# Kernel tuning notes

Measured on AMD Instinct MI355X. Metric: run time of the kernel, lower is better.

## Reference

```python
import jax, jax.numpy as jnp
import numpy as np

ANG_Y, ANG_X = 3, 3
ST = ANG_Y * ANG_X
K = 9                      # square kernel
OH, OW = 128, 128          # output_size
IN_C, OUT_C = 3, 3
H, W = 384, 384
B = 4


def setup_inputs() -> dict:
    key = jax.random.key(0)
    k_lf, = jax.random.split(key, 1)
    lf = jax.random.uniform(k_lf, (B, ST, IN_C, H, W), dtype=jnp.float32)
    # Learned locally-connected weights: one (out_c, in_c, OH, OW, K*K) tensor
    # per angular position, initialized as the center-tap identity (as in __init__).
    weights = jnp.zeros((ST, OUT_C, IN_C, OH, OW, K * K), dtype=jnp.float32)
    center = (K * K) // 2
    ch = jnp.arange(IN_C)
    weights = weights.at[:, ch, ch, :, :, center].set(1.0)
    biases = jnp.zeros((ST, OUT_C, OH, OW), dtype=jnp.float32)
    return {"lf": lf, "weights": weights, "biases": biases}


def reference(lf, weights, biases):
    b, st, c, h, w = lf.shape
    dh, dw = ANG_Y, ANG_X  # unfold stride
    # Padding exactly as in linear_filter
    pad_x = (OW - 1) * ANG_X + (K - w)
    pad_right = pad_x // 2
    pad_left = pad_x - pad_right
    pad_y = (OH - 1) * ANG_Y + (K - h)
    pad_bottom = pad_y // 2
    pad_top = pad_y - pad_bottom
    padded = jnp.pad(
        lf, ((0, 0), (0, 0), (0, 0), (pad_top, pad_bottom), (pad_left, pad_right))
    )
    # Extract K x K windows with stride (dh, dw), vectorized over batch and
    # all angular positions at once (replaces the triple Python loop).
    rows = jnp.arange(OH) * dh          # (OH,)
    cols = jnp.arange(OW) * dw          # (OW,)
    koff = jnp.arange(K)                # (K,)
    p = padded[:, :, :, rows[:, None] + koff[None, :], :]          # (b,st,c,OH,K,Wp)
    p = p[:, :, :, :, :, cols[:, None] + koff[None, :]]            # (b,st,c,OH,K,OW,K)
    p = p.transpose(0, 1, 2, 3, 5, 4, 6).reshape(b, st, c, OH, OW, K * K)
    # Locally-connected (unshared-weight) conv: per-angular, per-pixel weights.
    out = jnp.einsum("bsihwk,soihwk->bsohw", p, weights) + biases[None]
    return jnp.clip(out, 0.0, 1.0)
```

## Files before the change

### kernel.cpp

```cpp
#include <hip/hip_runtime.h>


#define ST 9
#define INC 3
#define OUTC 3
#define OHH 128
#define OWW 128
#define KDIM 9
#define KK 81
#define HH 384
#define WW 384
#define HWSZ (HH*WW)
#define WQ 16
#define SLICE (WQ*KK)

typedef float f32x4 __attribute__((ext_vector_type(4)));
struct __attribute__((packed, aligned(4))) U4 { f32x4 v; };

__device__ __forceinline__ void gll16(const float* g, float* l) {
  __builtin_amdgcn_global_load_lds((const __attribute__((address_space(1))) void*)g,
                                   (__attribute__((address_space(3))) void*)l, 16, 0, 0);
}

__global__ __launch_bounds__(128) void lf_filter_kernel(
    const float* __restrict__ lf, const float* __restrict__ wts,
    const float* __restrict__ bias, float* __restrict__ out)
{
  __shared__ __align__(16) float ldsW[OUTC][SLICE];

  const int t   = threadIdx.x;
  const int wl  = t & 15;
  const int b   = (t >> 4) & 3;
  const int kh  = t >> 6;
  const int bid = blockIdx.x;
  const int wg  = bid & 7;
  const int h   = (bid >> 3) & 127;
  const int s   = bid >> 10;
  const int w   = wg*WQ + wl;
  const int xbase = 3*w - 3;
  const int ybase = 3*h - 3;

  const int  base  = xbase < 0 ? 0 : (xbase > WW-KDIM ? WW-KDIM : xbase);
  const bool s_neg = (xbase < base);
  const bool s_pos = (xbase > base);

  const float* lfb = lf + (size_t)(b*ST + s)*INC*HWSZ;
  const int wu = (t & ~63) * 4;

  const int ky0 = kh ? 5 : 0;
  const int ky1 = kh ? 9 : 5;

  float acc[OUTC] = {0.f, 0.f, 0.f};

  #pragma unroll 1
  for (int i = 0; i < INC; ++i) {
    __syncthreads();

    #pragma unroll
    for (int o = 0; o < OUTC; ++o) {
      const float* wsrc = wts + ((size_t)(((s*OUTC + o)*INC + i)*OHH + h)*OWW + wg*WQ)*KK;
      float* dst = ldsW[o];
      #pragma unroll
      for (int j = 0; j < 2; ++j)
        gll16(wsrc + (size_t)(j*128 + t)*4, dst + j*512 + wu);
      if (t < 68)
        gll16(wsrc + (size_t)(256 + t)*4, dst + 1024 + wu);
    }
    __syncthreads();

    const float* lfr = lfb + (size_t)i*HWSZ;
    const int wb = wl*KK;
    #pragma unroll 1
    for (int ky = ky0; ky < ky1; ++ky) {
      const int y = ybase + ky;
      if ((unsigned)y < (unsigned)HH) {
        const float* rp = lfr + (size_t)y*WW + base;
        const f32x4 va = reinterpret_cast<const U4*>(rp)->v;
        const f32x4 vb = reinterpret_cast<const U4*>(rp + 4)->v;
        const float rc = rp[8];
        const float raw[KDIM] = {va.x, va.y, va.z, va.w, vb.x, vb.y, vb.z, vb.w, rc};
        float lv[KDIM];
        #pragma unroll
        for (int kx = 0; kx < KDIM; ++kx) {
          const float nv = (kx >= 3) ? raw[kx-3] : 0.f;
          const float pv = (kx <= 5) ? raw[kx+3] : 0.f;
          lv[kx] = s_neg ? nv : (s_pos ? pv : raw[kx]);
        }
        #pragma unroll
        for (int o = 0; o < OUTC; ++o) {
          const float* wrow = &ldsW[o][wb + ky*KDIM];
          float a = acc[o];
          #pragma unroll
          for (int kx = 0; kx < KDIM; ++kx)
            a = fmaf(lv[kx], wrow[kx], a);
          acc[o] = a;
        }
      }
    }
  }

  float* part = (float*)ldsW;
  __syncthreads();
  if (kh == 1) {
    const int q = t & 63;
    #pragma unroll
    for (int o = 0; o < OUTC; ++o) part[q*3 + o] = acc[o];
  }
  __syncthreads();
  if (kh == 0) {
    #pragma unroll
    for (int o = 0; o < OUTC; ++o) {
      const float bv = bias[((s*OUTC + o)*OHH + h)*OWW + w];
      float r = acc[o] + part[t*3 + o] + bv;
      r = r < 0.f ? 0.f : (r > 1.f ? 1.f : r);
      out[(((size_t)(b*ST + s)*OUTC + o)*OHH + h)*OWW + w] = r;
    }
  }
}

extern "C" void kernel_launch(void* const* d_in, const int* in_sizes, int n_in,
                              void* d_out, int out_size, void* d_ws, size_t ws_size,
                              hipStream_t stream) {
  const float* lf   = (const float*)d_in[0];
  const float* wts  = (const float*)d_in[1];
  const float* bias = (const float*)d_in[2];
  float* out = (float*)d_out;
  dim3 grid(ST * OHH * 8);
  dim3 block(128);
  hipLaunchKernelGGL(lf_filter_kernel, grid, block, 0, stream, lf, wts, bias, out);
}
```

Before: 99.97 us.

## Halve per-block width tile, split kernel rows four ways, and swizzle block order

Each block now covers 8 output columns instead of 16 and splits the 9 kernel rows across four thread groups (2,2,2,3) rather than two, doubling the grid. The LDS weight slice is halved and the cross-group reduction now sums three partial buffers. Block indices are also remapped so consecutive launched blocks stride across the grid, which spreads work and memory traffic across XCDs. The goal is more parallelism and shorter per-thread serial loops, at the cost of more blocks, more reduction traffic and less reuse of weight loads.

```diff
diff --git a/kernel.cpp b/kernel.cpp
--- a/kernel.cpp
+++ b/kernel.cpp
@@ -11,8 +11,9 @@
 #define HH 384
 #define WW 384
 #define HWSZ (HH*WW)
-#define WQ 16
+#define WQ 8
 #define SLICE (WQ*KK)
+#define NWG (ST*OHH*16)
 
 typedef float f32x4 __attribute__((ext_vector_type(4)));
 struct __attribute__((packed, aligned(4))) U4 { f32x4 v; };
@@ -29,13 +30,14 @@
   __shared__ __align__(16) float ldsW[OUTC][SLICE];
 
   const int t   = threadIdx.x;
-  const int wl  = t & 15;
-  const int b   = (t >> 4) & 3;
-  const int kh  = t >> 6;
-  const int bid = blockIdx.x;
-  const int wg  = bid & 7;
-  const int h   = (bid >> 3) & 127;
-  const int s   = bid >> 10;
+  const int wl  = t & 7;
+  const int b   = (t >> 3) & 3;
+  const int kq  = t >> 5;
+  const int raw = blockIdx.x;
+  const int bid = (raw & 7) * (NWG/8) + (raw >> 3);
+  const int wg  = bid & 15;
+  const int h   = (bid >> 4) & 127;
+  const int s   = bid >> 11;
   const int w   = wg*WQ + wl;
   const int xbase = 3*w - 3;
   const int ybase = 3*h - 3;
@@ -47,8 +49,8 @@
   const float* lfb = lf + (size_t)(b*ST + s)*INC*HWSZ;
   const int wu = (t & ~63) * 4;
 
-  const int ky0 = kh ? 5 : 0;
-  const int ky1 = kh ? 9 : 5;
+  const int kyA = kq*2;
+  const int nky = (kq == 3) ? 3 : 2;
 
   float acc[OUTC] = {0.f, 0.f, 0.f};
 
@@ -60,35 +62,35 @@
     for (int o = 0; o < OUTC; ++o) {
       const float* wsrc = wts + ((size_t)(((s*OUTC + o)*INC + i)*OHH + h)*OWW + wg*WQ)*KK;
       float* dst = ldsW[o];
-      #pragma unroll
-      for (int j = 0; j < 2; ++j)
-        gll16(wsrc + (size_t)(j*128 + t)*4, dst + j*512 + wu);
-      if (t < 68)
-        gll16(wsrc + (size_t)(256 + t)*4, dst + 1024 + wu);
+      gll16(wsrc + (size_t)t*4, dst + wu);
+      if (t < 34)
+        gll16(wsrc + (size_t)(128 + t)*4, dst + 512 + wu);
     }
     __syncthreads();
 
     const float* lfr = lfb + (size_t)i*HWSZ;
     const int wb = wl*KK;
     #pragma unroll 1
-    for (int ky = ky0; ky < ky1; ++ky) {
-      const int y = ybase + ky;
+    for (int r = 0; r < nky; ++r) {
+      const int ky = kyA + r;
+      const int y  = ybase + ky;
       if ((unsigned)y < (unsigned)HH) {
         const float* rp = lfr + (size_t)y*WW + base;
         const f32x4 va = reinterpret_cast<const U4*>(rp)->v;
         const f32x4 vb = reinterpret_cast<const U4*>(rp + 4)->v;
         const float rc = rp[8];
-        const float raw[KDIM] = {va.x, va.y, va.z, va.w, vb.x, vb.y, vb.z, vb.w, rc};
+        const float raw9[KDIM] = {va.x, va.y, va.z, va.w, vb.x, vb.y, vb.z, vb.w, rc};
         float lv[KDIM];
         #pragma unroll
         for (int kx = 0; kx < KDIM; ++kx) {
-          const float nv = (kx >= 3) ? raw[kx-3] : 0.f;
-          const float pv = (kx <= 5) ? raw[kx+3] : 0.f;
-          lv[kx] = s_neg ? nv : (s_pos ? pv : raw[kx]);
+          const float nv = (kx >= 3) ? raw9[kx-3] : 0.f;
+          const float pv = (kx <= 5) ? raw9[kx+3] : 0.f;
+          lv[kx] = s_neg ? nv : (s_pos ? pv : raw9[kx]);
         }
+        const int kb = wb + ky*KDIM;
         #pragma unroll
         for (int o = 0; o < OUTC; ++o) {
-          const float* wrow = &ldsW[o][wb + ky*KDIM];
+          const float* wrow = &ldsW[o][kb];
           float a = acc[o];
           #pragma unroll
           for (int kx = 0; kx < KDIM; ++kx)
@@ -101,17 +103,17 @@
 
   float* part = (float*)ldsW;
   __syncthreads();
-  if (kh == 1) {
-    const int q = t & 63;
+  if (kq != 0) {
+    const int q = t & 31;
     #pragma unroll
-    for (int o = 0; o < OUTC; ++o) part[q*3 + o] = acc[o];
+    for (int o = 0; o < OUTC; ++o) part[(kq-1)*96 + q*3 + o] = acc[o];
   }
   __syncthreads();
-  if (kh == 0) {
+  if (kq == 0) {
     #pragma unroll
     for (int o = 0; o < OUTC; ++o) {
       const float bv = bias[((s*OUTC + o)*OHH + h)*OWW + w];
-      float r = acc[o] + part[t*3 + o] + bv;
+      float r = acc[o] + part[t*3 + o] + part[96 + t*3 + o] + part[192 + t*3 + o] + bv;
       r = r < 0.f ? 0.f : (r > 1.f ? 1.f : r);
       out[(((size_t)(b*ST + s)*OUTC + o)*OHH + h)*OWW + w] = r;
     }
@@ -125,7 +127,7 @@
   const float* wts  = (const float*)d_in[1];
   const float* bias = (const float*)d_in[2];
   float* out = (float*)d_out;
-  dim3 grid(ST * OHH * 8);
+  dim3 grid(NWG);
   dim3 block(128);
   hipLaunchKernelGGL(lf_filter_kernel, grid, block, 0, stream, lf, wts, bias, out);
 }
```

Measured after the change: 109.9 us. 1.1x slower.
